# Kernel optimization log

Hardware: AMD Instinct MI355X
Metric: run time of the kernel (lower is better)

Reference implementation:

```python
import jax, jax.numpy as jnp
import numpy as np

G = 4            # group order (e.g., C4)
H = 16           # attention heads
DH = 64          # head dim
D = 1024         # token dim = H*DH = C*G
DI = 4096        # FFN inner dim
MAXREL = 32      # relative position clamp
EPS = 1e-5


def eq_ln(x):
    # Equivariant LayerNorm: (N, D) -> (N, G, D/G), LN over last dim, no affine
    N, Dt = x.shape
    xr = x.reshape(N, G, Dt // G)
    mu = jnp.mean(xr, axis=-1, keepdims=True)
    var = jnp.var(xr, axis=-1, keepdims=True)
    return ((xr - mu) * jax.lax.rsqrt(var + EPS)).reshape(N, Dt)


def ada_ln(x, temb, w, b):
    # AdaLN: scale/shift from SiLU(temb) -> Linear -> chunk
    n = eq_ln(x)
    ss = jax.nn.silu(temb) @ w.T + b                      # (N, 2D)
    scale, shift = jnp.split(ss, 2, axis=1)
    return n * (1.0 + scale) + shift


def attention(xq, xkv, wq, wk, wv, wo, bo, rel_table):
    # xq: (B,Tq,D), xkv: (B,Tk,D); rel_table: (H, 2*MAXREL+1) or None
    B, Tq, _ = xq.shape
    Tk = xkv.shape[1]
    q = (xq @ wq.T).reshape(B, Tq, H, DH)
    k = (xkv @ wk.T).reshape(B, Tk, H, DH)
    v = (xkv @ wv.T).reshape(B, Tk, H, DH)
    scores = jnp.einsum('bthd,bkhd->bhtk', q, k) * (DH ** -0.5)
    if rel_table is not None:
        rel_idx = jnp.clip(jnp.arange(Tq)[:, None] - jnp.arange(Tk)[None, :],
                           -MAXREL, MAXREL) + MAXREL      # (Tq, Tk)
        scores = scores + rel_table[:, rel_idx][None]     # (1,H,Tq,Tk)
    attn = jax.nn.softmax(scores, axis=-1)
    out = jnp.einsum('bhtk,bkhd->bthd', attn, v).reshape(B, Tq, H * DH)
    return out @ wo.T + bo


def setup_inputs() -> dict:
    key = jax.random.key(0)
    ks = jax.random.split(key, 24)
    s = 0.02
    B, T = 4, 1024
    inp = {
        'hidden_states': jax.random.normal(ks[0], (B, T, D), jnp.float32),
        'encoder_hidden_states': jax.random.normal(ks[1], (B, T, D), jnp.float32),
        'temb': jax.random.normal(ks[2], (B * T, D), jnp.float32),
        # AdaLN 1 / 2
        'w_ada1': jax.random.normal(ks[3], (2 * D, D), jnp.float32) * s,
        'b_ada1': jnp.zeros((2 * D,), jnp.float32),
        'w_ada2': jax.random.normal(ks[4], (2 * D, D), jnp.float32) * s,
        'b_ada2': jnp.zeros((2 * D,), jnp.float32),
        # self-attention (attention_bias=False, out_bias=True)
        'wq1': jax.random.normal(ks[5], (D, D), jnp.float32) * s,
        'wk1': jax.random.normal(ks[6], (D, D), jnp.float32) * s,
        'wv1': jax.random.normal(ks[7], (D, D), jnp.float32) * s,
        'wo1': jax.random.normal(ks[8], (D, D), jnp.float32) * s,
        'bo1': jnp.zeros((D,), jnp.float32),
        'rel_bias': jax.random.normal(ks[9], (H, 2 * MAXREL + 1), jnp.float32) * s,
        # cross-attention
        'wq2': jax.random.normal(ks[10], (D, D), jnp.float32) * s,
        'wk2': jax.random.normal(ks[11], (D, D), jnp.float32) * s,
        'wv2': jax.random.normal(ks[12], (D, D), jnp.float32) * s,
        'wo2': jax.random.normal(ks[13], (D, D), jnp.float32) * s,
        'bo2': jnp.zeros((D,), jnp.float32),
        # GEGLU FFN
        'w_ff1': jax.random.normal(ks[14], (2 * DI, D), jnp.float32) * s,
        'b_ff1': jnp.zeros((2 * DI,), jnp.float32),
        'w_ff2': jax.random.normal(ks[15], (D, DI), jnp.float32) * s,
        'b_ff2': jnp.zeros((D,), jnp.float32),
    }
    return inp


def reference(hidden_states, encoder_hidden_states, temb,
              w_ada1, b_ada1, w_ada2, b_ada2,
              wq1, wk1, wv1, wo1, bo1, rel_bias,
              wq2, wk2, wv2, wo2, bo2,
              w_ff1, b_ff1, w_ff2, b_ff2):
    B, T, Dm = hidden_states.shape
    x = hidden_states.reshape(B * T, Dm)
    # 1) AdaLN + self-attention with relative position bias + residual
    x1 = ada_ln(x, temb, w_ada1, b_ada1).reshape(B, T, Dm)
    x = x + attention(x1, x1, wq1, wk1, wv1, wo1, bo1, rel_bias).reshape(B * T, Dm)
    # 2) AdaLN + cross-attention + residual
    x2 = ada_ln(x, temb, w_ada2, b_ada2).reshape(B, T, Dm)
    x = x + attention(x2, encoder_hidden_states, wq2, wk2, wv2, wo2, bo2,
                      None).reshape(B * T, Dm)
    # 3) LayerNorm + GEGLU FFN + residual
    n3 = eq_ln(x)
    h12 = n3 @ w_ff1.T + b_ff1                            # (N, 2*DI)
    a, g = jnp.split(h12, 2, axis=-1)
    ff = (a * jax.nn.gelu(g, approximate=False)) @ w_ff2.T + b_ff2
    x = x + ff
    return x.reshape(B, T, Dm)
```

## Files before the change

kernel.cpp:

```cpp
#include <hip/hip_runtime.h>
#include <math.h>

typedef __attribute__((ext_vector_type(4))) float f32x4;
typedef __attribute__((ext_vector_type(8))) __bf16 bf16x8;

#define MFMA_BF16(a, b, c) __builtin_amdgcn_mfma_f32_16x16x32_bf16((a), (b), (c), 0, 0, 0)

static __device__ __forceinline__ unsigned short f2b(float f) {
  unsigned int u = __float_as_uint(f);
  return (unsigned short)((u + 0x7FFFu + ((u >> 16) & 1u)) >> 16);
}
static __device__ __forceinline__ float b2f(unsigned short h) {
  return __uint_as_float(((unsigned int)h) << 16);
}
static __device__ __forceinline__ unsigned short bcvt(float f) {
  __bf16 h = (__bf16)f;
  return __builtin_bit_cast(unsigned short, h);
}

static __device__ __forceinline__ void gll16(const void* g, void* l) {
  __builtin_amdgcn_global_load_lds((const __attribute__((address_space(1))) void*)g,
                                   (__attribute__((address_space(3))) void*)l, 16, 0, 0);
}

struct CvtArgs {
  const float* src[12];
  unsigned short* dst[12];
  int start[12];
};
__global__ __launch_bounds__(256) void f2b_multi(CvtArgs a) {
  const int bid = blockIdx.x;
  int s = 11;
#pragma unroll
  for (int i = 11; i >= 1; --i)
    if (bid < a.start[i]) s = i - 1;
  const size_t i4 = (size_t)(bid - a.start[s]) * 256 + threadIdx.x;
  const float4 v = *(const float4*)(a.src[s] + i4 * 4);
  ushort4 o;
  o.x = f2b(v.x); o.y = f2b(v.y); o.z = f2b(v.z); o.w = f2b(v.w);
  *(ushort4*)(a.dst[s] + i4 * 4) = o;
}

__global__ __launch_bounds__(256) void f2bperm_kernel(const float* __restrict__ src,
                                                      unsigned short* __restrict__ dst) {
  const int r = blockIdx.x;
  const int rr = r & 4095;
  const int dr = ((rr >> 4) << 5) | ((r >> 12) << 4) | (rr & 15);
  const int c = threadIdx.x * 4;
  const float4 v = *(const float4*)(src + (size_t)r * 1024 + c);
  ushort4 o;
  o.x = f2b(v.x); o.y = f2b(v.y); o.z = f2b(v.z); o.w = f2b(v.w);
  *(ushort4*)(dst + (size_t)dr * 1024 + c) = o;
}

__global__ __launch_bounds__(256) void silu_kernel(const float* __restrict__ src,
                                                   unsigned short* __restrict__ dst, int n) {
  const int i = (blockIdx.x * 256 + threadIdx.x) * 4;
  if (i >= n) return;
  const float4 v = *(const float4*)(src + i);
  ushort4 o;
  o.x = f2b(v.x / (1.f + expf(-v.x)));
  o.y = f2b(v.y / (1.f + expf(-v.y)));
  o.z = f2b(v.z / (1.f + expf(-v.z)));
  o.w = f2b(v.w / (1.f + expf(-v.w)));
  *(ushort4*)(dst + i) = o;
}

template <int ADA>
__global__ __launch_bounds__(256) void eqln_kernel(const float* __restrict__ x,
                                                   const unsigned short* __restrict__ ss,
                                                   unsigned short* __restrict__ outp) {
  const int n = blockIdx.x;
  const int tid = threadIdx.x;
  const int g = tid >> 6, lane = tid & 63;
  const size_t base = (size_t)n * 1024 + g * 256 + lane * 4;
  const float4 v = *(const float4*)(x + base);
  float s = v.x + v.y + v.z + v.w;
  float s2 = v.x * v.x + v.y * v.y + v.z * v.z + v.w * v.w;
#pragma unroll
  for (int m = 1; m < 64; m <<= 1) {
    s += __shfl_xor(s, m, 64);
    s2 += __shfl_xor(s2, m, 64);
  }
  const float mu = s * (1.f / 256.f);
  const float var = s2 * (1.f / 256.f) - mu * mu;
  const float rs = rsqrtf(var + 1e-5f);
  float o0 = (v.x - mu) * rs, o1 = (v.y - mu) * rs, o2 = (v.z - mu) * rs, o3 = (v.w - mu) * rs;
  if (ADA) {
    const size_t sb = (size_t)n * 4096 + g * 256 + lane * 4;
    const ushort4 scv = *(const ushort4*)(ss + sb);
    const ushort4 shv = *(const ushort4*)(ss + sb + 1024);
    o0 = o0 * (1.f + b2f(scv.x)) + b2f(shv.x);
    o1 = o1 * (1.f + b2f(scv.y)) + b2f(shv.y);
    o2 = o2 * (1.f + b2f(scv.z)) + b2f(shv.z);
    o3 = o3 * (1.f + b2f(scv.w)) + b2f(shv.w);
  }
  ushort4 ov;
  ov.x = f2b(o0); ov.y = f2b(o1); ov.z = f2b(o2); ov.w = f2b(o3);
  *(ushort4*)(outp + base) = ov;
}

__global__ __launch_bounds__(256) void vtrans_kernel(const unsigned short* __restrict__ v,
                                                     unsigned short* __restrict__ vt, int T,
                                                     int ld) {
  const int t0 = blockIdx.x * 64, h = blockIdx.y, b = blockIdx.z;
  __shared__ unsigned short tile[64][65];
  const int tid = threadIdx.x;
#pragma unroll
  for (int rr = 0; rr < 2; ++rr) {
    const int tok = rr * 32 + (tid >> 3);
    const int d8 = (tid & 7) * 8;
    const uint4 x = *(const uint4*)(v + (size_t)(b * T + t0 + tok) * ld + h * 64 + d8);
    const unsigned int* xs = (const unsigned int*)&x;
#pragma unroll
    for (int j = 0; j < 4; ++j) {
      tile[d8 + 2 * j][tok] = (unsigned short)(xs[j] & 0xffffu);
      tile[d8 + 2 * j + 1][tok] = (unsigned short)(xs[j] >> 16);
    }
  }
  __syncthreads();
#pragma unroll
  for (int rr = 0; rr < 2; ++rr) {
    const int d = rr * 32 + (tid >> 3);
    const int t8 = (tid & 7) * 8;
    uint4 ov;
    unsigned int* ou = (unsigned int*)&ov;
#pragma unroll
    for (int j = 0; j < 4; ++j)
      ou[j] = (unsigned int)tile[d][t8 + 2 * j] | ((unsigned int)tile[d][t8 + 2 * j + 1] << 16);
    *(uint4*)(vt + ((size_t)((b * 16 + h) * 64 + d)) * T + t0 + t8) = ov;
  }
}

template <int BM, int BIAS, int RES, int OUTMODE>
__global__ __launch_bounds__(256, 4) void gemm_nt(const unsigned short* __restrict__ A,
                                                  const unsigned short* __restrict__ Bw,
                                                  const float* __restrict__ bias,
                                                  const float* res, void* Cout,
                                                  int M, int N, int K) {
  constexpr int MB = BM / 32;
  __shared__ unsigned short As[BM * 64];
  __shared__ unsigned short Bs[128 * 64];
  const int m0 = blockIdx.x * BM, n0 = blockIdx.y * 128;
  const int tid = threadIdx.x, lane = tid & 63;
  const int wr = (tid >> 7) & 1, wc = (tid >> 6) & 1;
  const int lr = lane & 15, ls = lane >> 4;

  const f32x4 fz = {0.f, 0.f, 0.f, 0.f};
  f32x4 acc[MB][4];
#pragma unroll
  for (int m = 0; m < MB; ++m)
#pragma unroll
    for (int n = 0; n < 4; ++n) acc[m][n] = fz;

  for (int k0 = 0; k0 < K; k0 += 64) {
#pragma unroll
    for (int it = 0; it < BM / 32; ++it) {
      const int u = it * 256 + tid;
      const int row = u >> 3, gs = (u & 7) ^ (row & 7);
      gll16(A + (size_t)(m0 + row) * K + k0 + gs * 8, As + u * 8);
    }
#pragma unroll
    for (int it = 0; it < 4; ++it) {
      const int u = it * 256 + tid;
      const int row = u >> 3, gs = (u & 7) ^ (row & 7);
      gll16(Bw + (size_t)(n0 + row) * K + k0 + gs * 8, Bs + u * 8);
    }
    __syncthreads();
#pragma unroll
    for (int kk = 0; kk < 2; ++kk) {
      bf16x8 af[MB], bfr[4];
#pragma unroll
      for (int m = 0; m < MB; ++m) {
        const int row = wr * (BM / 2) + m * 16 + lr;
        const int slot = (kk * 4 + ls) ^ (row & 7);
        af[m] = *(const bf16x8*)(As + row * 64 + slot * 8);
      }
#pragma unroll
      for (int n = 0; n < 4; ++n) {
        const int col = wc * 64 + n * 16 + lr;
        const int slot = (kk * 4 + ls) ^ (col & 7);
        bfr[n] = *(const bf16x8*)(Bs + col * 64 + slot * 8);
      }
#pragma unroll
      for (int m = 0; m < MB; ++m)
#pragma unroll
        for (int n = 0; n < 4; ++n) acc[m][n] = MFMA_BF16(af[m], bfr[n], acc[m][n]);
    }
    __syncthreads();
  }

  if (OUTMODE == 2) {
    const int pn0 = n0 + wc * 64;
#pragma unroll
    for (int m = 0; m < MB; ++m) {
#pragma unroll
      for (int j = 0; j < 2; ++j) {
        const int ocol = (pn0 >> 1) + j * 16 + lr;
        const float ba = bias[ocol];
        const float bg = bias[(N >> 1) + ocol];
#pragma unroll
        for (int r = 0; r < 4; ++r) {
          const int row = m0 + wr * (BM / 2) + m * 16 + ls * 4 + r;
          const float a = acc[m][2 * j][r] + ba;
          const float g = acc[m][2 * j + 1][r] + bg;
          const float gl = 0.5f * g * (1.f + erff(g * 0.70710678118654752f));
          ((unsigned short*)Cout)[(size_t)row * (N >> 1) + ocol] = f2b(a * gl);
        }
      }
    }
    return;
  }
#pragma unroll
  for (int m = 0; m < MB; ++m) {
#pragma unroll
    for (int n = 0; n < 4; ++n) {
      const int col = n0 + wc * 64 + n * 16 + lr;
      float bv = 0.f;
      if (BIAS) bv = bias[col];
#pragma unroll
      for (int r = 0; r < 4; ++r) {
        const int row = m0 + wr * (BM / 2) + m * 16 + ls * 4 + r;
        float v = acc[m][n][r] + bv;
        if (RES) v += res[(size_t)row * N + col];
        if (OUTMODE == 1)
          ((unsigned short*)Cout)[(size_t)row * N + col] = f2b(v);
        else
          ((float*)Cout)[(size_t)row * N + col] = v;
      }
    }
  }
}

template <int RELB>
__global__ __launch_bounds__(256) void attn_kernel(const unsigned short* __restrict__ q,
                                                   const unsigned short* __restrict__ k,
                                                   const unsigned short* __restrict__ vt,
                                                   const float* __restrict__ rel,
                                                   unsigned short* __restrict__ outp,
                                                   int ldq, int ldk) {
  const int lin = blockIdx.x + (blockIdx.y << 4) + (blockIdx.z << 8);
  const int xcd = lin & 7, s = lin >> 3;
  const int g = (xcd << 3) + (s >> 4);
  const int qb = s & 15;
  const int h = g & 15, b = g >> 4;
  const int tid = threadIdx.x;
  const int wid = tid >> 6, lane = tid & 63;
  const int lr = lane & 15, ls = lane >> 4;
  const int q0 = (qb << 6) + (wid << 4);
  const float L2E = 1.44269504088896340736f;

  __shared__ unsigned short Ks[2][128 * 64];
  __shared__ unsigned short plds[4][16][64];
  __shared__ float tbl[66];

  if (RELB && tid < 65) tbl[tid] = rel[h * 65 + tid] * L2E;

  bf16x8 qa0, qa1;
  {
    const unsigned short* qp = q + (size_t)(b * 1024 + q0 + lr) * ldq + h * 64 + ls * 8;
    const bf16x8 t0 = *(const bf16x8*)qp;
    const bf16x8 t1 = *(const bf16x8*)(qp + 32);
    const float sc = 0.125f * L2E;
#pragma unroll
    for (int j = 0; j < 8; ++j) {
      qa0[j] = (__bf16)((float)t0[j] * sc);
      qa1[j] = (__bf16)((float)t1[j] * sc);
    }
  }
  bf16x8 ones;
#pragma unroll
  for (int j = 0; j < 8; ++j) ones[j] = (__bf16)1.0f;

  const f32x4 fz = {0.f, 0.f, 0.f, 0.f};
  f32x4 oacc[4];
#pragma unroll
  for (int d = 0; d < 4; ++d) oacc[d] = fz;
  f32x4 lacc = fz;

  const unsigned short* kbp = k + (size_t)(b * 1024) * ldk + h * 64;
  const unsigned short* vbp = vt + (size_t)((b * 16 + h) * 64) * 1024;

#pragma unroll
  for (int it = 0; it < 4; ++it) {
    const int u = it * 256 + tid;
    const int row = u >> 3, gs = (u & 7) ^ (row & 7);
    gll16(kbp + (size_t)row * ldk + gs * 8, Ks[0] + u * 8);
  }
  __syncthreads();

  for (int t = 0; t < 8; ++t) {
    const int kv0 = t << 7;
    bf16x8 vr[16];
#pragma unroll
    for (int hf = 0; hf < 2; ++hf)
#pragma unroll
      for (int d = 0; d < 4; ++d) {
        const unsigned short* vp = vbp + (size_t)(d * 16 + lr) * 1024 + kv0 + hf * 64 + ls * 8;
        vr[hf * 8 + 2 * d] = *(const bf16x8*)vp;
        vr[hf * 8 + 2 * d + 1] = *(const bf16x8*)(vp + 32);
      }
    if (t + 1 < 8) {
      const unsigned short* kst = kbp + (size_t)((t + 1) << 7) * ldk;
#pragma unroll
      for (int it = 0; it < 4; ++it) {
        const int u = it * 256 + tid;
        const int row = u >> 3, gs = (u & 7) ^ (row & 7);
        gll16(kst + (size_t)row * ldk + gs * 8, Ks[(t + 1) & 1] + u * 8);
      }
    }
    const unsigned short* kbuf = Ks[t & 1];
#pragma unroll
    for (int sub = 0; sub < 2; ++sub) {
      const int kvs = kv0 + sub * 64;
      f32x4 sc4[4];
      __builtin_amdgcn_s_setprio(1);
#pragma unroll
      for (int nn = 0; nn < 4; ++nn) {
        const int row = sub * 64 + nn * 16 + lr;
        const int s0 = ls ^ (row & 7), s1 = (4 + ls) ^ (row & 7);
        const bf16x8 kb0 = *(const bf16x8*)(kbuf + row * 64 + s0 * 8);
        const bf16x8 kb1 = *(const bf16x8*)(kbuf + row * 64 + s1 * 8);
        f32x4 acc = fz;
        acc = MFMA_BF16(qa0, kb0, acc);
        acc = MFMA_BF16(qa1, kb1, acc);
        sc4[nn] = acc;
      }
      __builtin_amdgcn_s_setprio(0);
      float cb = 0.f;
      bool vary = false;
      if (RELB) {
        if (kvs + 95 <= q0) {
          cb = tbl[64];
        } else if (kvs >= q0 + 47) {
          cb = tbl[0];
        } else {
          vary = true;
        }
      }
      if (vary) {
        const int bd = q0 + ls * 4 - (kvs + lr);
#pragma unroll
        for (int nn = 0; nn < 4; ++nn)
#pragma unroll
          for (int r = 0; r < 4; ++r) {
            int dl = bd + r - nn * 16;
            dl = dl < -32 ? -32 : (dl > 32 ? 32 : dl);
            const float p = __builtin_amdgcn_exp2f(fminf(sc4[nn][r] + tbl[dl + 32], 60.f));
            const int qq = ls * 4 + r;
            const int colw = ((((nn << 1) + (lr >> 3)) ^ (qq & 7)) << 3) + (lr & 7);
            plds[wid][qq][colw] = bcvt(p);
          }
      } else {
#pragma unroll
        for (int nn = 0; nn < 4; ++nn)
#pragma unroll
          for (int r = 0; r < 4; ++r) {
            const float p = __builtin_amdgcn_exp2f(fminf(sc4[nn][r] + cb, 60.f));
            const int qq = ls * 4 + r;
            const int colw = ((((nn << 1) + (lr >> 3)) ^ (qq & 7)) << 3) + (lr & 7);
            plds[wid][qq][colw] = bcvt(p);
          }
      }
      asm volatile("" ::: "memory");
      const bf16x8 pa0 = *(const bf16x8*)&plds[wid][lr][((ls ^ (lr & 7)) << 3)];
      const bf16x8 pa1 = *(const bf16x8*)&plds[wid][lr][(((4 + ls) ^ (lr & 7)) << 3)];
      __builtin_amdgcn_s_setprio(1);
      lacc = MFMA_BF16(pa0, ones, lacc);
      lacc = MFMA_BF16(pa1, ones, lacc);
#pragma unroll
      for (int d = 0; d < 4; ++d) {
        oacc[d] = MFMA_BF16(pa0, vr[sub * 8 + 2 * d], oacc[d]);
        oacc[d] = MFMA_BF16(pa1, vr[sub * 8 + 2 * d + 1], oacc[d]);
      }
      __builtin_amdgcn_s_setprio(0);
    }
    __syncthreads();
  }

  float rinv[4];
#pragma unroll
  for (int r = 0; r < 4; ++r) rinv[r] = 1.0f / lacc[r];
#pragma unroll
  for (int d = 0; d < 4; ++d)
#pragma unroll
    for (int r = 0; r < 4; ++r) {
      const float v = oacc[d][r] * rinv[r];
      outp[(size_t)(b * 1024 + q0 + ls * 4 + r) * 1024 + h * 64 + d * 16 + lr] = bcvt(v);
    }
}

extern "C" void kernel_launch(void* const* d_in, const int* in_sizes, int n_in,
                              void* d_out, int out_size, void* d_ws, size_t ws_size,
                              hipStream_t stream) {
  (void)in_sizes; (void)n_in; (void)out_size; (void)ws_size;
  const float* hs = (const float*)d_in[0];
  const float* enc = (const float*)d_in[1];
  const float* temb = (const float*)d_in[2];
  const float* wada1 = (const float*)d_in[3];
  const float* bada1 = (const float*)d_in[4];
  const float* wada2 = (const float*)d_in[5];
  const float* bada2 = (const float*)d_in[6];
  const float* wq1 = (const float*)d_in[7];
  const float* wk1 = (const float*)d_in[8];
  const float* wv1 = (const float*)d_in[9];
  const float* wo1 = (const float*)d_in[10];
  const float* bo1 = (const float*)d_in[11];
  const float* rel = (const float*)d_in[12];
  const float* wq2 = (const float*)d_in[13];
  const float* wk2 = (const float*)d_in[14];
  const float* wv2 = (const float*)d_in[15];
  const float* wo2 = (const float*)d_in[16];
  const float* bo2 = (const float*)d_in[17];
  const float* wff1 = (const float*)d_in[18];
  const float* bff1 = (const float*)d_in[19];
  const float* wff2 = (const float*)d_in[20];
  const float* bff2 = (const float*)d_in[21];
  float* out = (float*)d_out;

  char* ws = (char*)d_ws;
  const size_t MB = 1024ull * 1024ull;
  unsigned short* wb_ada = (unsigned short*)(ws + 0 * MB);
  unsigned short* wb_q1 = (unsigned short*)(ws + 8 * MB);
  unsigned short* wb_k1 = (unsigned short*)(ws + 10 * MB);
  unsigned short* wb_v1 = (unsigned short*)(ws + 12 * MB);
  unsigned short* wb_o1 = (unsigned short*)(ws + 14 * MB);
  unsigned short* wb_q2 = (unsigned short*)(ws + 16 * MB);
  unsigned short* wb_k2 = (unsigned short*)(ws + 18 * MB);
  unsigned short* wb_v2 = (unsigned short*)(ws + 20 * MB);
  unsigned short* wb_o2 = (unsigned short*)(ws + 22 * MB);
  unsigned short* wb_ff1 = (unsigned short*)(ws + 24 * MB);
  unsigned short* wb_ff2 = (unsigned short*)(ws + 40 * MB);
  unsigned short* silu_t = (unsigned short*)(ws + 48 * MB);
  unsigned short* enc_b = (unsigned short*)(ws + 56 * MB);
  unsigned short* ssb = (unsigned short*)(ws + 64 * MB);
  unsigned short* ffin = (unsigned short*)(ws + 64 * MB);
  float* bias_cat = (float*)(ws + 96 * MB);
  unsigned short* x1b = (unsigned short*)(ws + 97 * MB);
  unsigned short* qkvb = (unsigned short*)(ws + 105 * MB);
  unsigned short* qb = (unsigned short*)(ws + 105 * MB);
  unsigned short* kvb = (unsigned short*)(ws + 113 * MB);
  unsigned short* vtb = (unsigned short*)(ws + 129 * MB);
  unsigned short* aob = (unsigned short*)(ws + 137 * MB);

  const int Nrow = 4096;

  {
    CvtArgs a;
    const float* srcs[12] = {wada1, wada2, wq1, wk1, wv1, wo1, wq2, wk2, wv2, wo2, wff2, enc};
    unsigned short* dsts[12] = {wb_ada, wb_ada + 2048 * 1024, wb_q1, wb_k1, wb_v1, wb_o1,
                                wb_q2, wb_k2, wb_v2, wb_o2, wb_ff2, enc_b};
    const int blks[12] = {2048, 2048, 1024, 1024, 1024, 1024, 1024, 1024, 1024, 1024, 4096, 4096};
    int acc = 0;
    for (int i = 0; i < 12; ++i) { a.src[i] = srcs[i]; a.dst[i] = dsts[i]; a.start[i] = acc; acc += blks[i]; }
    f2b_multi<<<acc, 256, 0, stream>>>(a);
  }
  hipMemcpyAsync(bias_cat, bada1, 2048 * sizeof(float), hipMemcpyDeviceToDevice, stream);
  hipMemcpyAsync(bias_cat + 2048, bada2, 2048 * sizeof(float), hipMemcpyDeviceToDevice, stream);
  f2bperm_kernel<<<8192, 256, 0, stream>>>(wff1, wb_ff1);
  silu_kernel<<<4096, 256, 0, stream>>>(temb, silu_t, 4096 * 1024);

  gemm_nt<128, 1, 0, 1><<<dim3(32, 32), 256, 0, stream>>>(silu_t, wb_ada, bias_cat, nullptr, ssb, Nrow, 4096, 1024);

  eqln_kernel<1><<<4096, 256, 0, stream>>>(hs, ssb, x1b);
  gemm_nt<128, 0, 0, 1><<<dim3(32, 24), 256, 0, stream>>>(x1b, wb_q1, nullptr, nullptr, qkvb, Nrow, 3072, 1024);
  vtrans_kernel<<<dim3(16, 16, 4), 256, 0, stream>>>(qkvb + 2048, vtb, 1024, 3072);
  attn_kernel<1><<<dim3(16, 16, 4), 256, 0, stream>>>(qkvb, qkvb + 1024, vtb, rel, aob, 3072, 3072);
  gemm_nt<64, 1, 1, 0><<<dim3(64, 8), 256, 0, stream>>>(aob, wb_o1, bo1, hs, out, Nrow, 1024, 1024);

  eqln_kernel<1><<<4096, 256, 0, stream>>>(out, ssb + 2048, x1b);
  gemm_nt<64, 0, 0, 1><<<dim3(64, 8), 256, 0, stream>>>(x1b, wb_q2, nullptr, nullptr, qb, Nrow, 1024, 1024);
  gemm_nt<128, 0, 0, 1><<<dim3(32, 16), 256, 0, stream>>>(enc_b, wb_k2, nullptr, nullptr, kvb, Nrow, 2048, 1024);
  vtrans_kernel<<<dim3(16, 16, 4), 256, 0, stream>>>(kvb + 1024, vtb, 1024, 2048);
  attn_kernel<0><<<dim3(16, 16, 4), 256, 0, stream>>>(qb, kvb, vtb, nullptr, aob, 1024, 2048);
  gemm_nt<64, 1, 1, 0><<<dim3(64, 8), 256, 0, stream>>>(aob, wb_o2, bo2, out, out, Nrow, 1024, 1024);

  eqln_kernel<0><<<4096, 256, 0, stream>>>(out, nullptr, x1b);
  gemm_nt<128, 1, 0, 2><<<dim3(32, 64), 256, 0, stream>>>(x1b, wb_ff1, bff1, nullptr, ffin, Nrow, 8192, 1024);
  gemm_nt<64, 1, 1, 0><<<dim3(64, 8), 256, 0, stream>>>(ffin, wb_ff2, bff2, out, out, Nrow, 1024, 4096);
}
```

Measured before the change: 486.1 us.

## Add 256x256-tile pipelined GEMM kernel for the large wide-N projections

Introduces a 512-thread GEMM with 256x256 output tiles, double-buffered LDS staging via global_load_lds, and prefetch of the next K-tile interleaved with MFMA phases under raised wave priority. It replaces the 128-row gemm_nt launches for the AdaLN scale/shift, fused QKV, and GEGLU FF1 projections, and moves the GEGLU epilogue into the new kernel. The goal is more data reuse per tile and overlap of global loads with compute. The cost is higher register and LDS pressure (128 KB LDS per block) and fewer blocks per GEMM, which may leave some CUs idle.

Measured after the change: 551.3 us. 13.4% more time.

```diff
diff --git a/kernel.cpp b/kernel.cpp
--- a/kernel.cpp
+++ b/kernel.cpp
@@ -190,27 +190,6 @@
     __syncthreads();
   }
 
-  if (OUTMODE == 2) {
-    const int pn0 = n0 + wc * 64;
-#pragma unroll
-    for (int m = 0; m < MB; ++m) {
-#pragma unroll
-      for (int j = 0; j < 2; ++j) {
-        const int ocol = (pn0 >> 1) + j * 16 + lr;
-        const float ba = bias[ocol];
-        const float bg = bias[(N >> 1) + ocol];
-#pragma unroll
-        for (int r = 0; r < 4; ++r) {
-          const int row = m0 + wr * (BM / 2) + m * 16 + ls * 4 + r;
-          const float a = acc[m][2 * j][r] + ba;
-          const float g = acc[m][2 * j + 1][r] + bg;
-          const float gl = 0.5f * g * (1.f + erff(g * 0.70710678118654752f));
-          ((unsigned short*)Cout)[(size_t)row * (N >> 1) + ocol] = f2b(a * gl);
-        }
-      }
-    }
-    return;
-  }
 #pragma unroll
   for (int m = 0; m < MB; ++m) {
 #pragma unroll
@@ -227,6 +206,135 @@
           ((unsigned short*)Cout)[(size_t)row * N + col] = f2b(v);
         else
           ((float*)Cout)[(size_t)row * N + col] = v;
+      }
+    }
+  }
+}
+
+template <int BIAS, int OUTMODE>
+__global__ __launch_bounds__(512, 2) void gemm256(const unsigned short* __restrict__ A,
+                                                  const unsigned short* __restrict__ Bw,
+                                                  const float* __restrict__ bias,
+                                                  void* Cout, int M, int N, int K) {
+  __shared__ unsigned short As[2 * 16384];
+  __shared__ unsigned short Bs[2 * 16384];
+  const int m0 = blockIdx.x * 256, n0 = blockIdx.y * 256;
+  const int tid = threadIdx.x, lane = tid & 63;
+  const int wid = tid >> 6;
+  const int wr = wid >> 2, wc = wid & 3;
+  const int lr = lane & 15, ls = lane >> 4;
+
+  const f32x4 fz = {0.f, 0.f, 0.f, 0.f};
+  f32x4 acc[8][4];
+#pragma unroll
+  for (int m = 0; m < 8; ++m)
+#pragma unroll
+    for (int n = 0; n < 4; ++n) acc[m][n] = fz;
+
+  auto stage = [&](unsigned short* dst, const unsigned short* src, int rowbase, int h, int k0) {
+#pragma unroll
+    for (int it = 0; it < 2; ++it) {
+      const int u = it * 512 + tid;
+      const int rl = u >> 3;
+      const int gs = (u & 7) ^ (rl & 7);
+      gll16(src + (size_t)(rowbase + h * 128 + rl) * K + k0 + gs * 8, dst + h * 8192 + u * 8);
+    }
+  };
+
+  const int NT = K >> 6;
+  stage(As, A, m0, 0, 0);
+  stage(As, A, m0, 1, 0);
+  stage(Bs, Bw, n0, 0, 0);
+  stage(Bs, Bw, n0, 1, 0);
+  asm volatile("s_waitcnt vmcnt(0)" ::: "memory");
+  __builtin_amdgcn_s_barrier();
+
+  for (int kt = 0; kt < NT; ++kt) {
+    const int cur = (kt & 1) * 16384;
+    const int nxtb = ((kt & 1) ^ 1) * 16384;
+    const int kn = (kt + 1) << 6;
+    const bool pre = (kt + 1 < NT);
+    bf16x8 bfr[4][2];
+    bf16x8 af[2][2];
+
+#pragma unroll
+    for (int p = 0; p < 4; ++p) {
+      if (p == 0) {
+#pragma unroll
+        for (int n = 0; n < 4; ++n) {
+          const int row = wc * 64 + n * 16 + lr;
+#pragma unroll
+          for (int kk = 0; kk < 2; ++kk) {
+            const int slot = (kk * 4 + ls) ^ (row & 7);
+            bfr[n][kk] = *(const bf16x8*)(Bs + cur + row * 64 + slot * 8);
+          }
+        }
+      }
+#pragma unroll
+      for (int mm = 0; mm < 2; ++mm) {
+        const int row = wr * 128 + (2 * p + mm) * 16 + lr;
+#pragma unroll
+        for (int kk = 0; kk < 2; ++kk) {
+          const int slot = (kk * 4 + ls) ^ (row & 7);
+          af[mm][kk] = *(const bf16x8*)(As + cur + row * 64 + slot * 8);
+        }
+      }
+      if (pre) {
+        if (p == 0) {
+          stage(As + nxtb, A, m0, 0, kn);
+          stage(As + nxtb, A, m0, 1, kn);
+        } else if (p == 1) {
+          stage(Bs + nxtb, Bw, n0, 0, kn);
+          stage(Bs + nxtb, Bw, n0, 1, kn);
+        }
+      }
+      __builtin_amdgcn_s_barrier();
+      __builtin_amdgcn_s_setprio(1);
+#pragma unroll
+      for (int mm = 0; mm < 2; ++mm)
+#pragma unroll
+        for (int kk = 0; kk < 2; ++kk)
+#pragma unroll
+          for (int n = 0; n < 4; ++n)
+            acc[2 * p + mm][n] = MFMA_BF16(af[mm][kk], bfr[n][kk], acc[2 * p + mm][n]);
+      __builtin_amdgcn_s_setprio(0);
+      if (p == 3) asm volatile("s_waitcnt vmcnt(0)" ::: "memory");
+      __builtin_amdgcn_s_barrier();
+    }
+  }
+
+  if (OUTMODE == 2) {
+    const int pn0 = n0 + wc * 64;
+#pragma unroll
+    for (int m = 0; m < 8; ++m) {
+#pragma unroll
+      for (int j = 0; j < 2; ++j) {
+        const int ocol = (pn0 >> 1) + j * 16 + lr;
+        const float ba = bias[ocol];
+        const float bg = bias[(N >> 1) + ocol];
+#pragma unroll
+        for (int r = 0; r < 4; ++r) {
+          const int row = m0 + wr * 128 + m * 16 + ls * 4 + r;
+          const float a = acc[m][2 * j][r] + ba;
+          const float g = acc[m][2 * j + 1][r] + bg;
+          const float gl = 0.5f * g * (1.f + erff(g * 0.70710678118654752f));
+          ((unsigned short*)Cout)[(size_t)row * (N >> 1) + ocol] = f2b(a * gl);
+        }
+      }
+    }
+    return;
+  }
+#pragma unroll
+  for (int m = 0; m < 8; ++m) {
+#pragma unroll
+    for (int n = 0; n < 4; ++n) {
+      const int col = n0 + wc * 64 + n * 16 + lr;
+      float bv = 0.f;
+      if (BIAS) bv = bias[col];
+#pragma unroll
+      for (int r = 0; r < 4; ++r) {
+        const int row = m0 + wr * 128 + m * 16 + ls * 4 + r;
+        ((unsigned short*)Cout)[(size_t)row * N + col] = f2b(acc[m][n][r] + bv);
       }
     }
   }
@@ -455,15 +563,15 @@
     for (int i = 0; i < 12; ++i) { a.src[i] = srcs[i]; a.dst[i] = dsts[i]; a.start[i] = acc; acc += blks[i]; }
     f2b_multi<<<acc, 256, 0, stream>>>(a);
   }
-  hipMemcpyAsync(bias_cat, bada1, 2048 * sizeof(float), hipMemcpyDeviceToDevice, stream);
-  hipMemcpyAsync(bias_cat + 2048, bada2, 2048 * sizeof(float), hipMemcpyDeviceToDevice, stream);
+  (void)hipMemcpyAsync(bias_cat, bada1, 2048 * sizeof(float), hipMemcpyDeviceToDevice, stream);
+  (void)hipMemcpyAsync(bias_cat + 2048, bada2, 2048 * sizeof(float), hipMemcpyDeviceToDevice, stream);
   f2bperm_kernel<<<8192, 256, 0, stream>>>(wff1, wb_ff1);
   silu_kernel<<<4096, 256, 0, stream>>>(temb, silu_t, 4096 * 1024);
 
-  gemm_nt<128, 1, 0, 1><<<dim3(32, 32), 256, 0, stream>>>(silu_t, wb_ada, bias_cat, nullptr, ssb, Nrow, 4096, 1024);
+  gemm256<1, 1><<<dim3(16, 16), 512, 0, stream>>>(silu_t, wb_ada, bias_cat, ssb, Nrow, 4096, 1024);
 
   eqln_kernel<1><<<4096, 256, 0, stream>>>(hs, ssb, x1b);
-  gemm_nt<128, 0, 0, 1><<<dim3(32, 24), 256, 0, stream>>>(x1b, wb_q1, nullptr, nullptr, qkvb, Nrow, 3072, 1024);
+  gemm256<0, 1><<<dim3(16, 12), 512, 0, stream>>>(x1b, wb_q1, nullptr, qkvb, Nrow, 3072, 1024);
   vtrans_kernel<<<dim3(16, 16, 4), 256, 0, stream>>>(qkvb + 2048, vtb, 1024, 3072);
   attn_kernel<1><<<dim3(16, 16, 4), 256, 0, stream>>>(qkvb, qkvb + 1024, vtb, rel, aob, 3072, 3072);
   gemm_nt<64, 1, 1, 0><<<dim3(64, 8), 256, 0, stream>>>(aob, wb_o1, bo1, hs, out, Nrow, 1024, 1024);
@@ -476,6 +584,6 @@
   gemm_nt<64, 1, 1, 0><<<dim3(64, 8), 256, 0, stream>>>(aob, wb_o2, bo2, out, out, Nrow, 1024, 1024);
 
   eqln_kernel<0><<<4096, 256, 0, stream>>>(out, nullptr, x1b);
-  gemm_nt<128, 1, 0, 2><<<dim3(32, 64), 256, 0, stream>>>(x1b, wb_ff1, bff1, nullptr, ffin, Nrow, 8192, 1024);
+  gemm256<1, 2><<<dim3(16, 32), 512, 0, stream>>>(x1b, wb_ff1, bff1, ffin, Nrow, 8192, 1024);
   gemm_nt<64, 1, 1, 0><<<dim3(64, 8), 256, 0, stream>>>(ffin, wb_ff2, bff2, out, out, Nrow, 1024, 4096);
 }
```
